# Kernel optimization log

Measured on AMD Instinct MI355X. Metric: run time of the kernel, lower is better.

## Reference

```python
import jax, jax.numpy as jnp
import numpy as np

B, C_IN, IMG, P = 64, 3, 224, 16
GRID = IMG // P              # 14
N_PATCH = GRID * GRID        # 196
S = N_PATCH + 1              # 197 tokens incl CLS
D, H, HD = 768, 12, 64
DFF = 3072
L, PRUNE_AFTER = 12, 4
RATIO, EPS = 0.5, 1e-6
NEG = -1e30                  # additive mask value (softmax weight -> exactly 0 in fp32)
N_CLASSES = 1000
N_KEEP = max(1, int(S * (1.0 - RATIO)))  # 98, matches torch topk count


def _ln(x, g, b):
    m = x.mean(-1, keepdims=True)
    v = ((x - m) ** 2).mean(-1, keepdims=True)
    return (x - m) * jax.lax.rsqrt(v + EPS) * g + b


def _attn(x, qkv_w, qkv_b, proj_w, proj_b, amask):
    Bx, N, C = x.shape
    qkv = (x @ qkv_w.T + qkv_b).reshape(Bx, N, 3, H, HD).transpose(2, 0, 3, 1, 4)
    q, k, v = qkv[0], qkv[1], qkv[2]            # [B,H,N,HD]
    s = jnp.einsum('bhqd,bhkd->bhqk', q, k) * (HD ** -0.5)
    if amask is not None:
        s = s + amask                            # [B,1,1,N] broadcast
    a = jax.nn.softmax(s, axis=-1)
    o = jnp.einsum('bhqk,bhkd->bhqd', a, v).transpose(0, 2, 1, 3).reshape(Bx, N, C)
    return o @ proj_w.T + proj_b


def _block(x, i, p, amask=None):
    h = _ln(x, p['ln1_g'][i], p['ln1_b'][i])
    x = x + _attn(h, p['qkv_w'][i], p['qkv_b'][i], p['proj_w'][i], p['proj_b'][i], amask)
    h = _ln(x, p['ln2_g'][i], p['ln2_b'][i])
    h = jax.nn.gelu(h @ p['fc1_w'][i].T + p['fc1_b'][i], approximate=False)
    x = x + (h @ p['fc2_w'][i].T + p['fc2_b'][i])
    return x


def _forward(images, patch_w, patch_b, cls_token, pos_embed,
             ln1_g, ln1_b, qkv_w, qkv_b, proj_w, proj_b,
             ln2_g, ln2_b, fc1_w, fc1_b, fc2_w, fc2_b,
             norm_g, norm_b, head_w, head_b):
    p = dict(ln1_g=ln1_g, ln1_b=ln1_b, qkv_w=qkv_w, qkv_b=qkv_b,
             proj_w=proj_w, proj_b=proj_b, ln2_g=ln2_g, ln2_b=ln2_b,
             fc1_w=fc1_w, fc1_b=fc1_b, fc2_w=fc2_w, fc2_b=fc2_b)
    Bx = images.shape[0]
    # patch embed: non-overlapping 16x16 conv == patch extract + matmul
    patches = images.reshape(Bx, C_IN, GRID, P, GRID, P).transpose(0, 2, 4, 1, 3, 5)
    patches = patches.reshape(Bx, N_PATCH, C_IN * P * P)
    x = patches @ patch_w.reshape(D, -1).T + patch_b          # [B,196,768]
    x = jnp.concatenate([jnp.broadcast_to(cls_token, (Bx, 1, D)), x], axis=1)
    x = x + pos_embed                                          # [B,197,768]
    # early dense blocks
    for i in range(PRUNE_AFTER):
        x = _block(x, i, p)
    # _threshold_prune: topk on token norms, CLS always kept
    scores = jnp.linalg.norm(x, axis=-1)                       # [B,S]
    _, idx = jax.lax.top_k(scores, N_KEEP)                     # [B,98]
    mask = jnp.zeros((Bx, S), bool).at[jnp.arange(Bx)[:, None], idx].set(True)
    mask = mask.at[:, 0].set(True)
    # _gather_pad: kept tokens compacted to front (original order), zeros after
    order = jnp.argsort(~mask, axis=1, stable=True)            # True positions first
    x_pad = jnp.take_along_axis(x, order[:, :, None], axis=1)
    attn_m = jnp.take_along_axis(mask, order, axis=1)          # [B,S] True-prefix
    x_pad = x_pad * attn_m[:, :, None]
    amask = jnp.where(attn_m, 0.0, NEG).astype(x.dtype)[:, None, None, :]  # [B,1,1,S]
    # late masked blocks
    for i in range(PRUNE_AFTER, L):
        x_pad = _block(x_pad, i, p, amask)
    cls = _ln(x_pad[:, 0], norm_g, norm_b)
    return cls @ head_w.T + head_b                             # [B,1000]


def setup_inputs():
    key = jax.random.key(0)
    ks = iter(jax.random.split(key, 32))
    r = lambda shape: jax.random.normal(next(ks), shape, jnp.float32) * 0.02
    return {
        'images': jax.random.normal(next(ks), (B, C_IN, IMG, IMG), jnp.float32),
        'patch_w': r((D, C_IN, P, P)),
        'patch_b': r((D,)),
        'cls_token': r((1, 1, D)),
        'pos_embed': r((1, S, D)),
        'ln1_g': jnp.ones((L, D), jnp.float32),
        'ln1_b': jnp.zeros((L, D), jnp.float32),
        'qkv_w': r((L, 3 * D, D)),
        'qkv_b': r((L, 3 * D)),
        'proj_w': r((L, D, D)),
        'proj_b': r((L, D)),
        'ln2_g': jnp.ones((L, D), jnp.float32),
        'ln2_b': jnp.zeros((L, D), jnp.float32),
        'fc1_w': r((L, DFF, D)),
        'fc1_b': r((L, DFF)),
        'fc2_w': r((L, D, DFF)),
        'fc2_b': r((L, D)),
        'norm_g': jnp.ones((D,), jnp.float32),
        'norm_b': jnp.zeros((D,), jnp.float32),
        'head_w': r((N_CLASSES, D)),
        'head_b': r((N_CLASSES,)),
    }


def reference(images, patch_w, patch_b, cls_token, pos_embed,
              ln1_g, ln1_b, qkv_w, qkv_b, proj_w, proj_b,
              ln2_g, ln2_b, fc1_w, fc1_b, fc2_w, fc2_b,
              norm_g, norm_b, head_w, head_b):
    return _forward(images, patch_w, patch_b, cls_token, pos_embed,
                    ln1_g, ln1_b, qkv_w, qkv_b, proj_w, proj_b,
                    ln2_g, ln2_b, fc1_w, fc1_b, fc2_w, fc2_b,
                    norm_g, norm_b, head_w, head_b)
```

## Files before the change

kernel.cpp:

```cpp
#include <hip/hip_runtime.h>
#include <cstdint>
#include <cstddef>


#define NTOK 197
#define NB 64
#define NHEAD 12
#define SL 99

typedef __attribute__((ext_vector_type(8))) _Float16 half8;
typedef __attribute__((ext_vector_type(4))) float f32x4;
typedef __attribute__((ext_vector_type(4))) unsigned short us4;

#define DEV static __device__ __forceinline__

DEV unsigned short f2h(float f) {
    union { _Float16 h; unsigned short u; } v;
    v.h = (_Float16)f;
    return v.u;
}
DEV float h2f(unsigned short u) {
    union { _Float16 h; unsigned short u; } v;
    v.u = u;
    return (float)v.h;
}

DEV void gload16(const void* g, void* l) {
    __builtin_amdgcn_global_load_lds((const __attribute__((address_space(1))) unsigned int*)g,
                                     (__attribute__((address_space(3))) unsigned int*)l, 16, 0, 0);
}

DEV float gelu_f(float v) {
    float x = v * 0.70710678118654752f;
    float ax = fabsf(x);
    float t = __builtin_amdgcn_rcpf(fmaf(0.3275911f, ax, 1.0f));
    float poly = fmaf(fmaf(fmaf(fmaf(1.061405429f, t, -1.453152027f), t,
                               1.421413741f), t, -0.284496736f), t, 0.254829592f) * t;
    float erf_ax = 1.0f - poly * __expf(-x * x);
    float er = (x < 0.f) ? -erf_ax : erf_ax;
    return 0.5f * v * (1.0f + er);
}

__global__ __launch_bounds__(256) void cvt_layer4_k(const float* __restrict__ qw,
                                                    const float* __restrict__ pw,
                                                    const float* __restrict__ f1,
                                                    const float* __restrict__ f2,
                                                    int i0,
                                                    unsigned short* __restrict__ dst)
{
    int l = blockIdx.x / 6912;
    int b2 = blockIdx.x % 6912;
    int li = i0 + l;
    size_t t = (size_t)b2 * 256 + threadIdx.x;
    size_t e = t * 4;
    const float* src; size_t loc;
    if (e < 1769472)      { src = qw + (size_t)li * 1769472; loc = e; }
    else if (e < 2359296) { src = pw + (size_t)li * 589824;  loc = e - 1769472; }
    else if (e < 4718592) { src = f1 + (size_t)li * 2359296; loc = e - 2359296; }
    else                  { src = f2 + (size_t)li * 2359296; loc = e - 4718592; }
    float4 v = *(const float4*)(src + loc);
    us4 hi; hi.x = f2h(v.x); hi.y = f2h(v.y); hi.z = f2h(v.z); hi.w = f2h(v.w);
    *(us4*)(dst + (size_t)l * 7077888 + e) = hi;
}

__global__ __launch_bounds__(256) void cvt_simple_k(const float* __restrict__ src,
                                                    unsigned short* __restrict__ dh, int n4)
{
    int t = blockIdx.x * 256 + threadIdx.x;
    if (t >= n4) return;
    size_t e = (size_t)t * 4;
    float4 v = *(const float4*)(src + e);
    us4 hi; hi.x = f2h(v.x); hi.y = f2h(v.y); hi.z = f2h(v.z); hi.w = f2h(v.w);
    *(us4*)(dh + e) = hi;
}

__global__ __launch_bounds__(256) void patch_extract2_k(const float* __restrict__ img,
                                                        unsigned short* __restrict__ ph)
{
    int pi = blockIdx.x, b = blockIdx.y;
    int gy = pi / 14, gx = pi % 14;
    size_t obase = ((size_t)b * 196 + pi) * 768;
    for (int f = threadIdx.x; f < 768; f += 256) {
        int c = f >> 8, py = (f >> 4) & 15, px = f & 15;
        float v = img[(((size_t)b * 3 + c) * 224 + gy * 16 + py) * 224 + gx * 16 + px];
        ph[obase + f] = f2h(v);
    }
}

__global__ __launch_bounds__(256) void assemble_k(const unsigned short* __restrict__ emb,
                                                  const float* __restrict__ cls,
                                                  const float* __restrict__ pos,
                                                  unsigned short* __restrict__ x)
{
    int s = blockIdx.x, b = blockIdx.y;
    size_t xo = ((size_t)b * NTOK + s) * 768;
    for (int d = threadIdx.x; d < 768; d += 256) {
        float v = (s == 0) ? cls[d] : h2f(emb[((size_t)b * 196 + (s - 1)) * 768 + d]);
        x[xo + d] = f2h(v + pos[(size_t)s * 768 + d]);
    }
}

__global__ __launch_bounds__(64) void lnw_k(const unsigned short* __restrict__ in,
                                            unsigned short* __restrict__ outh,
                                            const float* __restrict__ g,
                                            const float* __restrict__ bt, size_t ldin)
{
    const unsigned short* xr = in + (size_t)blockIdx.x * ldin;
    size_t ob = (size_t)blockIdx.x * 768;
    const int t = threadIdx.x;
    const int e0 = t * 12;

    us4 a = *(const us4*)(xr + e0);
    us4 b = *(const us4*)(xr + e0 + 4);
    us4 c = *(const us4*)(xr + e0 + 8);
    float v[12];
    v[0] = h2f(a.x); v[1] = h2f(a.y); v[2]  = h2f(a.z); v[3]  = h2f(a.w);
    v[4] = h2f(b.x); v[5] = h2f(b.y); v[6]  = h2f(b.z); v[7]  = h2f(b.w);
    v[8] = h2f(c.x); v[9] = h2f(c.y); v[10] = h2f(c.z); v[11] = h2f(c.w);

    float s = 0.f;
#pragma unroll
    for (int e = 0; e < 12; e++) s += v[e];
#pragma unroll
    for (int o = 32; o; o >>= 1) s += __shfl_xor(s, o);
    float mean = s * (1.f / 768.f);
    float ss = 0.f;
#pragma unroll
    for (int e = 0; e < 12; e++) { float d = v[e] - mean; ss += d * d; }
#pragma unroll
    for (int o = 32; o; o >>= 1) ss += __shfl_xor(ss, o);
    float inv = rsqrtf(ss * (1.f / 768.f) + 1e-6f);

    float4 g0 = *(const float4*)(g + e0),  g1 = *(const float4*)(g + e0 + 4),  g2 = *(const float4*)(g + e0 + 8);
    float4 b0 = *(const float4*)(bt + e0), b1 = *(const float4*)(bt + e0 + 4), b2 = *(const float4*)(bt + e0 + 8);
    float gg[12] = {g0.x,g0.y,g0.z,g0.w, g1.x,g1.y,g1.z,g1.w, g2.x,g2.y,g2.z,g2.w};
    float bb[12] = {b0.x,b0.y,b0.z,b0.w, b1.x,b1.y,b1.z,b1.w, b2.x,b2.y,b2.z,b2.w};
    unsigned short o16[12];
#pragma unroll
    for (int e = 0; e < 12; e++) o16[e] = f2h((v[e] - mean) * inv * gg[e] + bb[e]);
    us4 oa = {o16[0], o16[1], o16[2],  o16[3]};
    us4 obv = {o16[4], o16[5], o16[6],  o16[7]};
    us4 oc = {o16[8], o16[9], o16[10], o16[11]};
    *(us4*)(outh + ob + e0)     = oa;
    *(us4*)(outh + ob + e0 + 4) = obv;
    *(us4*)(outh + ob + e0 + 8) = oc;
}

template<int EPI, int OS, int MAP>
__global__ __launch_bounds__(256) void mgemm_k(const unsigned short* __restrict__ Ah,
                                               const unsigned short* __restrict__ Wh,
                                               const float* __restrict__ bias,
                                               const unsigned short* __restrict__ res,
                                               unsigned short* __restrict__ Chi,
                                               float* __restrict__ Cf,
                                               int M, int N, int K, int nR, int nC, int nRloc)
{
    __shared__ unsigned short lds[3 * 8192];

    int rt, ct;
    {
        int bid = blockIdx.x;
        if (MAP == 0) { rt = bid % nR; ct = bid / nR; }
        else {
            int xcd = bid & 7, u = bid >> 3, rl, c;
            if (MAP == 3) { rl = u % nRloc; c = u / nRloc; }
            else          { c = u % nC;     rl = u / nC;   }
            rt = xcd * nRloc + rl; ct = c;
            if (rt >= nR) return;
        }
    }
    const int row0 = rt << 7, col0 = ct << 7;
    const int tid = threadIdx.x;
    const int w = tid >> 6, lane = tid & 63;
    const int wr = w >> 1, wc = w & 1;
    const int srow = lane >> 2;
    const int schunk = ((lane & 3) ^ ((srow >> 1) & 3)) << 3;
    const int fr = lane & 15, fq = lane >> 4;
    const int rchunk = (fq ^ ((fr >> 1) & 3)) << 3;

    f32x4 acc[4][4];
#pragma unroll
    for (int m = 0; m < 4; m++)
#pragma unroll
        for (int n = 0; n < 4; n++) acc[m][n] = (f32x4)0.f;

    const int nk = K >> 5;

    auto stage = [&](int t, int slot) {
        const int k0 = t << 5;
        unsigned short* Ad = lds + slot * 8192;
        unsigned short* Bd = Ad + 4096;
#pragma unroll
        for (int i = 0; i < 2; i++) {
            int r = i * 64 + w * 16 + srow;
            int ga = row0 + r; if (ga > M - 1) ga = M - 1;
            int gb = col0 + r; if (gb > N - 1) gb = N - 1;
            gload16(Ah + (size_t)ga * K + k0 + schunk, Ad + i * 2048 + w * 512);
            gload16(Wh + (size_t)gb * K + k0 + schunk, Bd + i * 2048 + w * 512);
        }
    };

    stage(0, 0);
    stage(1, 1);
    int slot = 0, slot2 = 2;
    for (int t = 0; t < nk; ++t) {
        if (t + 1 < nk) asm volatile("s_waitcnt vmcnt(4)" ::: "memory");
        else            asm volatile("s_waitcnt vmcnt(0)" ::: "memory");
        __builtin_amdgcn_s_barrier();
        if (t + 2 < nk) stage(t + 2, slot2);
        const unsigned short* Ab = lds + slot * 8192;
        const unsigned short* Bb = Ab + 4096;
        half8 a[4], bb[4];
#pragma unroll
        for (int m = 0; m < 4; m++)
            a[m] = *(const half8*)(Ab + (wr * 64 + m * 16 + fr) * 32 + rchunk);
#pragma unroll
        for (int n = 0; n < 4; n++)
            bb[n] = *(const half8*)(Bb + (wc * 64 + n * 16 + fr) * 32 + rchunk);
#pragma unroll
        for (int m = 0; m < 4; m++)
#pragma unroll
            for (int n = 0; n < 4; n++)
                acc[m][n] = __builtin_amdgcn_mfma_f32_16x16x32_f16(a[m], bb[n], acc[m][n], 0, 0, 0);
        slot = (slot == 2) ? 0 : slot + 1;
        slot2 = (slot2 == 2) ? 0 : slot2 + 1;
    }

#pragma unroll
    for (int m = 0; m < 4; m++) {
#pragma unroll
        for (int n = 0; n < 4; n++) {
            int col = col0 + wc * 64 + n * 16 + fr;
#pragma unroll
            for (int r = 0; r < 4; r++) {
                int row = row0 + wr * 64 + m * 16 + fq * 4 + r;
                if (row < M && col < N) {
                    float v = acc[m][n][r] + bias[col];
                    size_t o = (size_t)row * N + col;
                    if (EPI == 2) v += h2f(res[o]);
                    if (EPI == 1) v = gelu_f(v);
                    if (OS == 0) Cf[o] = v;
                    else Chi[o] = f2h(v);
                }
            }
        }
    }
}

template<int S, int KT, int PVKT, int PSTR>
__global__ __launch_bounds__(256) void attn2_k(const unsigned short* __restrict__ qh,
                                               unsigned short* __restrict__ oh,
                                               const int* __restrict__ cntp)
{
    constexpr int PVK = PVKT * 32;
    constexpr int QT = (S + 15) / 16;
    extern __shared__ unsigned short sh[];
    unsigned short* VT = sh;
    unsigned short* PL = sh + 64 * PSTR;

    const int h = blockIdx.x, b = blockIdx.y;
    const int tid = threadIdx.x, w = tid >> 6, lane = tid & 63;
    const int nk = cntp ? cntp[b] : S;
    const size_t qbase = (size_t)b * S * 2304 + (size_t)h * 64;
    const int fr = lane & 15, fq = lane >> 4;

    for (int j0 = 0; j0 < S; j0 += 32) {
        int j = j0 + (tid >> 3);
        int d8 = (tid & 7) * 8;
        if (j < S) {
            size_t src = qbase + (size_t)j * 2304 + 1536 + d8;
            us4 v0 = *(const us4*)(qh + src);
            us4 v1 = *(const us4*)(qh + src + 4);
            VT[(d8 + 0) * PSTR + j] = v0.x; VT[(d8 + 1) * PSTR + j] = v0.y;
            VT[(d8 + 2) * PSTR + j] = v0.z; VT[(d8 + 3) * PSTR + j] = v0.w;
            VT[(d8 + 4) * PSTR + j] = v1.x; VT[(d8 + 5) * PSTR + j] = v1.y;
            VT[(d8 + 6) * PSTR + j] = v1.z; VT[(d8 + 7) * PSTR + j] = v1.w;
        }
    }
    for (int idx = tid; idx < 64 * (PVK - S); idx += 256) {
        int d = idx / (PVK - S), j = S + idx % (PVK - S);
        VT[d * PSTR + j] = 0;
    }
    {
        unsigned short* Pw = PL + w * 16 * PSTR;
        for (int idx = lane; idx < 16 * (PVK - 16 * KT); idx += 64) {
            int rr = idx / (PVK - 16 * KT), cc = 16 * KT + idx % (PVK - 16 * KT);
            Pw[rr * PSTR + cc] = 0;
        }
    }
    __syncthreads();

    for (int qt = w; qt < QT; qt += 4) {
        int qr = qt * 16 + fr; int qrc = qr < S ? qr : S - 1;
        const size_t qrow = qbase + (size_t)qrc * 2304;
        half8 qf0[2];
#pragma unroll
        for (int ks = 0; ks < 2; ks++)
            qf0[ks] = *(const half8*)(qh + qrow + ks * 32 + fq * 8);
        f32x4 sc[KT];
        __builtin_amdgcn_s_setprio(1);
#pragma unroll
        for (int kt = 0; kt < KT; kt++) {
            int ky = kt * 16 + fr; int kyc = ky < S ? ky : S - 1;
            const size_t krow = qbase + (size_t)kyc * 2304 + 768;
            f32x4 acc = (f32x4)0.f;
#pragma unroll
            for (int ks = 0; ks < 2; ks++) {
                half8 kh = *(const half8*)(qh + krow + ks * 32 + fq * 8);
                acc = __builtin_amdgcn_mfma_f32_16x16x32_f16(qf0[ks], kh, acc, 0, 0, 0);
            }
            sc[kt] = acc;
        }
        __builtin_amdgcn_s_setprio(0);
        float mx[4] = {-3e38f, -3e38f, -3e38f, -3e38f};
#pragma unroll
        for (int kt = 0; kt < KT; kt++) {
            bool valid = (kt * 16 + fr) < nk;
#pragma unroll
            for (int r = 0; r < 4; r++) {
                float s = sc[kt][r] * 0.125f;
                sc[kt][r] = s;
                if (valid) mx[r] = fmaxf(mx[r], s);
            }
        }
#pragma unroll
        for (int off = 1; off < 16; off <<= 1)
#pragma unroll
            for (int r = 0; r < 4; r++) mx[r] = fmaxf(mx[r], __shfl_xor(mx[r], off));
        float sum[4] = {0.f, 0.f, 0.f, 0.f};
#pragma unroll
        for (int kt = 0; kt < KT; kt++) {
            bool valid = (kt * 16 + fr) < nk;
#pragma unroll
            for (int r = 0; r < 4; r++) {
                float p = valid ? __expf(sc[kt][r] - mx[r]) : 0.f;
                sc[kt][r] = p;
                sum[r] += p;
            }
        }
#pragma unroll
        for (int off = 1; off < 16; off <<= 1)
#pragma unroll
            for (int r = 0; r < 4; r++) sum[r] += __shfl_xor(sum[r], off);
        float inv[4];
#pragma unroll
        for (int r = 0; r < 4; r++) inv[r] = 1.f / sum[r];
        unsigned short* Pw = PL + w * 16 * PSTR;
#pragma unroll
        for (int kt = 0; kt < KT; kt++) {
#pragma unroll
            for (int r = 0; r < 4; r++)
                Pw[(fq * 4 + r) * PSTR + kt * 16 + fr] = f2h(sc[kt][r] * inv[r]);
        }
        f32x4 o[4];
#pragma unroll
        for (int n = 0; n < 4; n++) o[n] = (f32x4)0.f;
        __builtin_amdgcn_s_setprio(1);
#pragma unroll
        for (int ks = 0; ks < PVKT; ks++) {
            half8 pa = *(const half8*)(Pw + fr * PSTR + ks * 32 + fq * 8);
#pragma unroll
            for (int n = 0; n < 4; n++) {
                half8 vb = *(const half8*)(VT + (n * 16 + fr) * PSTR + ks * 32 + fq * 8);
                o[n] = __builtin_amdgcn_mfma_f32_16x16x32_f16(pa, vb, o[n], 0, 0, 0);
            }
        }
        __builtin_amdgcn_s_setprio(0);
#pragma unroll
        for (int n = 0; n < 4; n++) {
#pragma unroll
            for (int r = 0; r < 4; r++) {
                int row = qt * 16 + fq * 4 + r;
                if (row < S) {
                    size_t oidx = ((size_t)b * S + row) * 768 + (size_t)h * 64 + n * 16 + fr;
                    oh[oidx] = f2h(o[n][r]);
                }
            }
        }
    }
}

__global__ __launch_bounds__(64) void normsq_k(const unsigned short* __restrict__ x,
                                               float* __restrict__ norms)
{
    const unsigned short* xr = x + (size_t)blockIdx.x * 768;
    const int t = threadIdx.x;
    const int e0 = t * 12;
    us4 a = *(const us4*)(xr + e0);
    us4 b = *(const us4*)(xr + e0 + 4);
    us4 c = *(const us4*)(xr + e0 + 8);
    float ss = 0.f;
    float v;
    v = h2f(a.x); ss += v * v; v = h2f(a.y); ss += v * v;
    v = h2f(a.z); ss += v * v; v = h2f(a.w); ss += v * v;
    v = h2f(b.x); ss += v * v; v = h2f(b.y); ss += v * v;
    v = h2f(b.z); ss += v * v; v = h2f(b.w); ss += v * v;
    v = h2f(c.x); ss += v * v; v = h2f(c.y); ss += v * v;
    v = h2f(c.z); ss += v * v; v = h2f(c.w); ss += v * v;
#pragma unroll
    for (int o = 32; o; o >>= 1) ss += __shfl_xor(ss, o);
    if (t == 0) norms[blockIdx.x] = ss;
}

__global__ __launch_bounds__(256) void topk_k(const float* __restrict__ norms,
                                              int* __restrict__ idxmap, int* __restrict__ cnt)
{
    int b = blockIdx.x, t = threadIdx.x;
    __shared__ float n[NTOK];
    __shared__ unsigned char kp[NTOK];
    if (t < NTOK) n[t] = norms[b * NTOK + t];
    __syncthreads();
    if (t < NTOK) {
        float me = n[t];
        int rank = 0;
        for (int j = 0; j < NTOK; j++) rank += (n[j] > me) || (n[j] == me && j < t);
        kp[t] = (rank < 98) || (t == 0);
    }
    __syncthreads();
    if (t == 0) {
        int c = 0;
        for (int s = 0; s < NTOK; s++) if (kp[s]) idxmap[b * SL + c++] = s;
        cnt[b] = c;
        for (int j = c; j < SL; j++) idxmap[b * SL + j] = 0;
    }
}

__global__ __launch_bounds__(64) void gather_k(const unsigned short* __restrict__ x,
                                               const int* __restrict__ idxmap,
                                               const int* __restrict__ cnt,
                                               unsigned short* __restrict__ xl)
{
    int j = blockIdx.x, b = blockIdx.y;
    size_t dst = ((size_t)b * SL + j) * 768;
    const int t = threadIdx.x;
    const int e0 = t * 12;
    if (j < cnt[b]) {
        int s = idxmap[b * SL + j];
        size_t src = ((size_t)b * NTOK + s) * 768;
        *(us4*)(xl + dst + e0)     = *(const us4*)(x + src + e0);
        *(us4*)(xl + dst + e0 + 4) = *(const us4*)(x + src + e0 + 4);
        *(us4*)(xl + dst + e0 + 8) = *(const us4*)(x + src + e0 + 8);
    } else {
        us4 z = {0, 0, 0, 0};
        *(us4*)(xl + dst + e0)     = z;
        *(us4*)(xl + dst + e0 + 4) = z;
        *(us4*)(xl + dst + e0 + 8) = z;
    }
}

extern "C" void kernel_launch(void* const* d_in, const int* in_sizes, int n_in,
                              void* d_out, int out_size, void* d_ws, size_t ws_size,
                              hipStream_t stream)
{
    const float* images  = (const float*)d_in[0];
    const float* patch_w = (const float*)d_in[1];
    const float* patch_b = (const float*)d_in[2];
    const float* cls_tok = (const float*)d_in[3];
    const float* pos_emb = (const float*)d_in[4];
    const float* ln1_g   = (const float*)d_in[5];
    const float* ln1_b   = (const float*)d_in[6];
    const float* qkv_w   = (const float*)d_in[7];
    const float* qkv_b   = (const float*)d_in[8];
    const float* proj_w  = (const float*)d_in[9];
    const float* proj_b  = (const float*)d_in[10];
    const float* ln2_g   = (const float*)d_in[11];
    const float* ln2_b   = (const float*)d_in[12];
    const float* fc1_w   = (const float*)d_in[13];
    const float* fc1_b   = (const float*)d_in[14];
    const float* fc2_w   = (const float*)d_in[15];
    const float* fc2_b   = (const float*)d_in[16];
    const float* norm_g  = (const float*)d_in[17];
    const float* norm_b  = (const float*)d_in[18];
    const float* head_w  = (const float*)d_in[19];
    const float* head_b  = (const float*)d_in[20];
    float* outp = (float*)d_out;

    char* W = (char*)d_ws;
    unsigned short* x16  = (unsigned short*)W;
    unsigned short* hbh  = (unsigned short*)(W + 19365888);
    char* R = W + 38731776;
    unsigned short* ph   = (unsigned short*)R;
    unsigned short* emb  = (unsigned short*)(R + 19365888);
    unsigned short* qkh  = (unsigned short*)R;
    unsigned short* ffh  = (unsigned short*)R;
    unsigned short* xl16 = (unsigned short*)(W + 116195328);
    unsigned short* wb4  = (unsigned short*)(W + 125927424);
    unsigned short* pwh  = (unsigned short*)(W + 182550528);
    unsigned short* hwb  = (unsigned short*)(W + 183730176);
    float* norms         = (float*)(W + 185303040);
    unsigned short* clsb = (unsigned short*)(W + 185353472);
    int* idxmap          = (int*)(W + 185451776);
    int* cnt             = (int*)(W + 185477120);

    const int LDS_EARLY = (64 * 232 + 4 * 16 * 232) * 2;
    const int LDS_LATE  = (64 * 136 + 4 * 16 * 136) * 2;
    (void)hipFuncSetAttribute(reinterpret_cast<const void*>(&attn2_k<197, 13, 7, 232>),
                              hipFuncAttributeMaxDynamicSharedMemorySize, LDS_EARLY);
    (void)hipFuncSetAttribute(reinterpret_cast<const void*>(&attn2_k<99, 7, 4, 136>),
                              hipFuncAttributeMaxDynamicSharedMemorySize, LDS_LATE);

    const int nR1 = 99, nRl1 = 13;
    const int nRp = 98, nRlp = 13;
    const int nR2 = 50, nRl2 = 7;

    cvt_simple_k<<<576, 256, 0, stream>>>(patch_w, pwh, 147456);
    patch_extract2_k<<<dim3(196, NB), 256, 0, stream>>>(images, ph);
    mgemm_k<0, 1, 3><<<8 * nRlp * 6, 256, 0, stream>>>(ph, pwh, patch_b, nullptr,
        emb, nullptr, 12544, 768, 768, nRp, 6, nRlp);
    assemble_k<<<dim3(NTOK, NB), 256, 0, stream>>>(emb, cls_tok, pos_emb, x16);

    const int M1 = NB * NTOK;
    for (int i = 0; i < 4; i++) {
        if (i == 0)
            cvt_layer4_k<<<4 * 6912, 256, 0, stream>>>(qkv_w, proj_w, fc1_w, fc2_w, 0, wb4);
        unsigned short* wbh = wb4 + (size_t)(i & 3) * 7077888;
        lnw_k<<<M1, 64, 0, stream>>>(x16, hbh, ln1_g + (size_t)i * 768, ln1_b + (size_t)i * 768, 768);
        mgemm_k<0, 1, 3><<<8 * nRl1 * 18, 256, 0, stream>>>(hbh, wbh,
            qkv_b + (size_t)i * 2304, nullptr, qkh, nullptr, M1, 2304, 768, nR1, 18, nRl1);
        attn2_k<197, 13, 7, 232><<<dim3(NHEAD, NB), 256, LDS_EARLY, stream>>>(qkh, hbh, nullptr);
        mgemm_k<2, 1, 3><<<8 * nRl1 * 6, 256, 0, stream>>>(hbh, wbh + 1769472,
            proj_b + (size_t)i * 768, x16, x16, nullptr, M1, 768, 768, nR1, 6, nRl1);
        lnw_k<<<M1, 64, 0, stream>>>(x16, hbh, ln2_g + (size_t)i * 768, ln2_b + (size_t)i * 768, 768);
        mgemm_k<1, 1, 3><<<8 * nRl1 * 24, 256, 0, stream>>>(hbh, wbh + 2359296,
            fc1_b + (size_t)i * 3072, nullptr, ffh, nullptr, M1, 3072, 768, nR1, 24, nRl1);
        mgemm_k<2, 1, 4><<<8 * nRl1 * 6, 256, 0, stream>>>(ffh, wbh + 4718592,
            fc2_b + (size_t)i * 768, x16, x16, nullptr, M1, 768, 3072, nR1, 6, nRl1);
    }

    normsq_k<<<M1, 64, 0, stream>>>(x16, norms);
    topk_k<<<NB, 256, 0, stream>>>(norms, idxmap, cnt);
    gather_k<<<dim3(SL, NB), 64, 0, stream>>>(x16, idxmap, cnt, xl16);

    const int M2 = NB * SL;
    for (int i = 4; i < 12; i++) {
        if (i == 4)
            cvt_layer4_k<<<4 * 6912, 256, 0, stream>>>(qkv_w, proj_w, fc1_w, fc2_w, 4, wb4);
        if (i == 8)
            cvt_layer4_k<<<4 * 6912, 256, 0, stream>>>(qkv_w, proj_w, fc1_w, fc2_w, 8, wb4);
        unsigned short* wbh = wb4 + (size_t)(i & 3) * 7077888;
        lnw_k<<<M2, 64, 0, stream>>>(xl16, hbh, ln1_g + (size_t)i * 768, ln1_b + (size_t)i * 768, 768);
        mgemm_k<0, 1, 3><<<8 * nRl2 * 18, 256, 0, stream>>>(hbh, wbh,
            qkv_b + (size_t)i * 2304, nullptr, qkh, nullptr, M2, 2304, 768, nR2, 18, nRl2);
        attn2_k<99, 7, 4, 136><<<dim3(NHEAD, NB), 256, LDS_LATE, stream>>>(qkh, hbh, cnt);
        mgemm_k<2, 1, 3><<<8 * nRl2 * 6, 256, 0, stream>>>(hbh, wbh + 1769472,
            proj_b + (size_t)i * 768, xl16, xl16, nullptr, M2, 768, 768, nR2, 6, nRl2);
        lnw_k<<<M2, 64, 0, stream>>>(xl16, hbh, ln2_g + (size_t)i * 768, ln2_b + (size_t)i * 768, 768);
        mgemm_k<1, 1, 3><<<8 * nRl2 * 24, 256, 0, stream>>>(hbh, wbh + 2359296,
            fc1_b + (size_t)i * 3072, nullptr, ffh, nullptr, M2, 3072, 768, nR2, 24, nRl2);
        mgemm_k<2, 1, 4><<<8 * nRl2 * 6, 256, 0, stream>>>(ffh, wbh + 4718592,
            fc2_b + (size_t)i * 768, xl16, xl16, nullptr, M2, 768, 3072, nR2, 6, nRl2);
    }

    lnw_k<<<NB, 64, 0, stream>>>(xl16, clsb, norm_g, norm_b, (size_t)SL * 768);
    cvt_simple_k<<<750, 256, 0, stream>>>(head_w, hwb, 192000);
    mgemm_k<0, 0, 0><<<8, 256, 0, stream>>>(clsb, hwb,
        head_b, nullptr, nullptr, outp, 64, 1000, 768, 1, 8, 1);
}
```

Measured before the change: 3.732 ms.

## Fold LayerNorm into QKV and FC1 GEMMs via weight scaling and row statistics

Removes the standalone LayerNorm kernels before the QKV and FC1 GEMMs. The gamma scale is folded into the fp16 weights during conversion, and per-column weight sums plus a beta/gamma-derived bias correction are precomputed. The GEMMs now consume the raw residual stream, accumulate per-row sum and sum-of-squares with fdot2 during the K loop, and apply mean/rstd correction in the epilogue. This saves a read and write of the normalized activations per LN, but adds dot ops to the inner loop and computes variance as E[x²]−mean², which can lose accuracy. The beta/gamma ratio is zero whenever gamma is zero.

```diff
diff --git a/kernel.cpp b/kernel.cpp
--- a/kernel.cpp
+++ b/kernel.cpp
@@ -9,6 +9,7 @@
 #define SL 99
 
 typedef __attribute__((ext_vector_type(8))) _Float16 half8;
+typedef __attribute__((ext_vector_type(2))) _Float16 half2;
 typedef __attribute__((ext_vector_type(4))) float f32x4;
 typedef __attribute__((ext_vector_type(4))) unsigned short us4;
 
@@ -41,10 +42,35 @@
     return 0.5f * v * (1.0f + er);
 }
 
+__global__ __launch_bounds__(256) void cvt_simple_k(const float* __restrict__ src,
+                                                    unsigned short* __restrict__ dh, int n4)
+{
+    int t = blockIdx.x * 256 + threadIdx.x;
+    if (t >= n4) return;
+    size_t e = (size_t)t * 4;
+    float4 v = *(const float4*)(src + e);
+    us4 hi; hi.x = f2h(v.x); hi.y = f2h(v.y); hi.z = f2h(v.z); hi.w = f2h(v.w);
+    *(us4*)(dh + e) = hi;
+}
+
+__global__ __launch_bounds__(256) void ratio_k(const float* __restrict__ ln1_g, const float* __restrict__ ln1_b,
+                                               const float* __restrict__ ln2_g, const float* __restrict__ ln2_b,
+                                               float* __restrict__ ratio)
+{
+    int idx = blockIdx.x * 256 + threadIdx.x;
+    if (idx >= 18432) return;
+    int l = idx / 1536, wh = (idx / 768) & 1, k = idx % 768;
+    float g = wh ? ln2_g[l * 768 + k] : ln1_g[l * 768 + k];
+    float b = wh ? ln2_b[l * 768 + k] : ln1_b[l * 768 + k];
+    ratio[idx] = (g != 0.f) ? b / g : 0.f;
+}
+
 __global__ __launch_bounds__(256) void cvt_layer4_k(const float* __restrict__ qw,
                                                     const float* __restrict__ pw,
                                                     const float* __restrict__ f1,
                                                     const float* __restrict__ f2,
+                                                    const float* __restrict__ ln1_g,
+                                                    const float* __restrict__ ln2_g,
                                                     int i0,
                                                     unsigned short* __restrict__ dst)
 {
@@ -54,24 +80,54 @@
     size_t t = (size_t)b2 * 256 + threadIdx.x;
     size_t e = t * 4;
     const float* src; size_t loc;
-    if (e < 1769472)      { src = qw + (size_t)li * 1769472; loc = e; }
+    const float* gsc = nullptr;
+    if (e < 1769472)      { src = qw + (size_t)li * 1769472; loc = e; gsc = ln1_g + (size_t)li * 768; }
     else if (e < 2359296) { src = pw + (size_t)li * 589824;  loc = e - 1769472; }
-    else if (e < 4718592) { src = f1 + (size_t)li * 2359296; loc = e - 2359296; }
+    else if (e < 4718592) { src = f1 + (size_t)li * 2359296; loc = e - 2359296; gsc = ln2_g + (size_t)li * 768; }
     else                  { src = f2 + (size_t)li * 2359296; loc = e - 4718592; }
     float4 v = *(const float4*)(src + loc);
+    if (gsc) {
+        int k = (int)(loc % 768);
+        float4 gv = *(const float4*)(gsc + k);
+        v.x *= gv.x; v.y *= gv.y; v.z *= gv.z; v.w *= gv.w;
+    }
     us4 hi; hi.x = f2h(v.x); hi.y = f2h(v.y); hi.z = f2h(v.z); hi.w = f2h(v.w);
     *(us4*)(dst + (size_t)l * 7077888 + e) = hi;
 }
 
-__global__ __launch_bounds__(256) void cvt_simple_k(const float* __restrict__ src,
-                                                    unsigned short* __restrict__ dh, int n4)
-{
-    int t = blockIdx.x * 256 + threadIdx.x;
-    if (t >= n4) return;
-    size_t e = (size_t)t * 4;
-    float4 v = *(const float4*)(src + e);
-    us4 hi; hi.x = f2h(v.x); hi.y = f2h(v.y); hi.z = f2h(v.z); hi.w = f2h(v.w);
-    *(us4*)(dh + e) = hi;
+__global__ __launch_bounds__(256) void sc_k(const unsigned short* __restrict__ wb4,
+                                            const float* __restrict__ ratio,
+                                            const float* __restrict__ qkv_b,
+                                            const float* __restrict__ fc1_b,
+                                            int i0,
+                                            float* __restrict__ sArr, float* __restrict__ cArr)
+{
+    int l = blockIdx.x / 1344;
+    int row = (blockIdx.x % 1344) * 4 + (threadIdx.x >> 6);
+    int lane = threadIdx.x & 63;
+    int li = i0 + l;
+    bool isq = row < 2304;
+    const unsigned short* wrow = wb4 + (size_t)l * 7077888 +
+        (isq ? (size_t)row * 768 : 2359296 + (size_t)(row - 2304) * 768);
+    const float* rat = ratio + ((size_t)li * 2 + (isq ? 0 : 1)) * 768;
+    float bias = isq ? qkv_b[(size_t)li * 2304 + row] : fc1_b[(size_t)li * 3072 + row - 2304];
+    int e0 = lane * 12;
+    us4 a = *(const us4*)(wrow + e0);
+    us4 b = *(const us4*)(wrow + e0 + 4);
+    us4 c = *(const us4*)(wrow + e0 + 8);
+    float4 r0 = *(const float4*)(rat + e0), r1 = *(const float4*)(rat + e0 + 4), r2 = *(const float4*)(rat + e0 + 8);
+    float v[12] = {h2f(a.x),h2f(a.y),h2f(a.z),h2f(a.w), h2f(b.x),h2f(b.y),h2f(b.z),h2f(b.w),
+                   h2f(c.x),h2f(c.y),h2f(c.z),h2f(c.w)};
+    float rr[12] = {r0.x,r0.y,r0.z,r0.w, r1.x,r1.y,r1.z,r1.w, r2.x,r2.y,r2.z,r2.w};
+    float s = 0.f, cc = 0.f;
+#pragma unroll
+    for (int e = 0; e < 12; e++) { s += v[e]; cc = fmaf(rr[e], v[e], cc); }
+#pragma unroll
+    for (int o = 32; o; o >>= 1) { s += __shfl_xor(s, o); cc += __shfl_xor(cc, o); }
+    if (lane == 0) {
+        sArr[(size_t)l * 5376 + row] = s;
+        cArr[(size_t)l * 5376 + row] = cc + bias;
+    }
 }
 
 __global__ __launch_bounds__(256) void patch_extract2_k(const float* __restrict__ img,
@@ -109,7 +165,6 @@
     size_t ob = (size_t)blockIdx.x * 768;
     const int t = threadIdx.x;
     const int e0 = t * 12;
-
     us4 a = *(const us4*)(xr + e0);
     us4 b = *(const us4*)(xr + e0 + 4);
     us4 c = *(const us4*)(xr + e0 + 8);
@@ -117,7 +172,6 @@
     v[0] = h2f(a.x); v[1] = h2f(a.y); v[2]  = h2f(a.z); v[3]  = h2f(a.w);
     v[4] = h2f(b.x); v[5] = h2f(b.y); v[6]  = h2f(b.z); v[7]  = h2f(b.w);
     v[8] = h2f(c.x); v[9] = h2f(c.y); v[10] = h2f(c.z); v[11] = h2f(c.w);
-
     float s = 0.f;
 #pragma unroll
     for (int e = 0; e < 12; e++) s += v[e];
@@ -130,7 +184,6 @@
 #pragma unroll
     for (int o = 32; o; o >>= 1) ss += __shfl_xor(ss, o);
     float inv = rsqrtf(ss * (1.f / 768.f) + 1e-6f);
-
     float4 g0 = *(const float4*)(g + e0),  g1 = *(const float4*)(g + e0 + 4),  g2 = *(const float4*)(g + e0 + 8);
     float4 b0 = *(const float4*)(bt + e0), b1 = *(const float4*)(bt + e0 + 4), b2 = *(const float4*)(bt + e0 + 8);
     float gg[12] = {g0.x,g0.y,g0.z,g0.w, g1.x,g1.y,g1.z,g1.w, g2.x,g2.y,g2.z,g2.w};
@@ -146,10 +199,11 @@
     *(us4*)(outh + ob + e0 + 8) = oc;
 }
 
-template<int EPI, int OS, int MAP>
+template<int EPI, int OS, int MAP, int LNF>
 __global__ __launch_bounds__(256) void mgemm_k(const unsigned short* __restrict__ Ah,
                                                const unsigned short* __restrict__ Wh,
                                                const float* __restrict__ bias,
+                                               const float* __restrict__ sArr,
                                                const unsigned short* __restrict__ res,
                                                unsigned short* __restrict__ Chi,
                                                float* __restrict__ Cf,
@@ -183,6 +237,10 @@
     for (int m = 0; m < 4; m++)
 #pragma unroll
         for (int n = 0; n < 4; n++) acc[m][n] = (f32x4)0.f;
+
+    float rs[4] = {0.f, 0.f, 0.f, 0.f};
+    float rq[4] = {0.f, 0.f, 0.f, 0.f};
+    const half2 one2 = {(_Float16)1.f, (_Float16)1.f};
 
     const int nk = K >> 5;
 
@@ -222,20 +280,57 @@
 #pragma unroll
             for (int n = 0; n < 4; n++)
                 acc[m][n] = __builtin_amdgcn_mfma_f32_16x16x32_f16(a[m], bb[n], acc[m][n], 0, 0, 0);
+        if (LNF) {
+#pragma unroll
+            for (int m = 0; m < 4; m++) {
+                const half2* p = (const half2*)&a[m];
+#pragma unroll
+                for (int j = 0; j < 4; j++) {
+                    rs[m] = __builtin_amdgcn_fdot2(p[j], one2, rs[m], false);
+                    rq[m] = __builtin_amdgcn_fdot2(p[j], p[j], rq[m], false);
+                }
+            }
+        }
         slot = (slot == 2) ? 0 : slot + 1;
         slot2 = (slot2 == 2) ? 0 : slot2 + 1;
     }
 
+    if (LNF) {
+#pragma unroll
+        for (int m = 0; m < 4; m++) {
+            rs[m] += __shfl_xor(rs[m], 16); rs[m] += __shfl_xor(rs[m], 32);
+            rq[m] += __shfl_xor(rq[m], 16); rq[m] += __shfl_xor(rq[m], 32);
+        }
+    }
+    const float invK = 1.f / (float)K;
+
 #pragma unroll
     for (int m = 0; m < 4; m++) {
+        float mean_r[4], rstd_r[4];
+        if (LNF) {
+#pragma unroll
+            for (int r = 0; r < 4; r++) {
+                int j = fq * 4 + r;
+                float sm = __shfl(rs[m], j);
+                float sq = __shfl(rq[m], j);
+                float mean = sm * invK;
+                float var = sq * invK - mean * mean;
+                mean_r[r] = mean;
+                rstd_r[r] = rsqrtf(var + 1e-6f);
+            }
+        }
 #pragma unroll
         for (int n = 0; n < 4; n++) {
             int col = col0 + wc * 64 + n * 16 + fr;
+            float sv = 0.f;
+            if (LNF && col < N) sv = sArr[col];
 #pragma unroll
             for (int r = 0; r < 4; r++) {
                 int row = row0 + wr * 64 + m * 16 + fq * 4 + r;
                 if (row < M && col < N) {
-                    float v = acc[m][n][r] + bias[col];
+                    float v;
+                    if (LNF) v = rstd_r[r] * (acc[m][n][r] - mean_r[r] * sv) + bias[col];
+                    else     v = acc[m][n][r] + bias[col];
                     size_t o = (size_t)row * N + col;
                     if (EPI == 2) v += h2f(res[o]);
                     if (EPI == 1) v = gelu_f(v);
@@ -491,6 +586,9 @@
     unsigned short* clsb = (unsigned short*)(W + 185353472);
     int* idxmap          = (int*)(W + 185451776);
     int* cnt             = (int*)(W + 185477120);
+    float* sArr          = (float*)(W + 185477632);
+    float* cArr          = (float*)(W + 185563648);
+    float* ratio         = (float*)(W + 185649664);
 
     const int LDS_EARLY = (64 * 232 + 4 * 16 * 232) * 2;
     const int LDS_LATE  = (64 * 136 + 4 * 16 * 136) * 2;
@@ -503,28 +601,32 @@
     const int nRp = 98, nRlp = 13;
     const int nR2 = 50, nRl2 = 7;
 
+    ratio_k<<<72, 256, 0, stream>>>(ln1_g, ln1_b, ln2_g, ln2_b, ratio);
+
     cvt_simple_k<<<576, 256, 0, stream>>>(patch_w, pwh, 147456);
     patch_extract2_k<<<dim3(196, NB), 256, 0, stream>>>(images, ph);
-    mgemm_k<0, 1, 3><<<8 * nRlp * 6, 256, 0, stream>>>(ph, pwh, patch_b, nullptr,
+    mgemm_k<0, 1, 3, 0><<<8 * nRlp * 6, 256, 0, stream>>>(ph, pwh, patch_b, nullptr, nullptr,
         emb, nullptr, 12544, 768, 768, nRp, 6, nRlp);
     assemble_k<<<dim3(NTOK, NB), 256, 0, stream>>>(emb, cls_tok, pos_emb, x16);
 
     const int M1 = NB * NTOK;
     for (int i = 0; i < 4; i++) {
-        if (i == 0)
-            cvt_layer4_k<<<4 * 6912, 256, 0, stream>>>(qkv_w, proj_w, fc1_w, fc2_w, 0, wb4);
+        if (i == 0) {
+            cvt_layer4_k<<<4 * 6912, 256, 0, stream>>>(qkv_w, proj_w, fc1_w, fc2_w, ln1_g, ln2_g, 0, wb4);
+            sc_k<<<4 * 1344, 256, 0, stream>>>(wb4, ratio, qkv_b, fc1_b, 0, sArr, cArr);
+        }
         unsigned short* wbh = wb4 + (size_t)(i & 3) * 7077888;
-        lnw_k<<<M1, 64, 0, stream>>>(x16, hbh, ln1_g + (size_t)i * 768, ln1_b + (size_t)i * 768, 768);
-        mgemm_k<0, 1, 3><<<8 * nRl1 * 18, 256, 0, stream>>>(hbh, wbh,
-            qkv_b + (size_t)i * 2304, nullptr, qkh, nullptr, M1, 2304, 768, nR1, 18, nRl1);
+        float* sL = sArr + (size_t)(i & 3) * 5376;
+        float* cL = cArr + (size_t)(i & 3) * 5376;
+        mgemm_k<0, 1, 3, 1><<<8 * nRl1 * 18, 256, 0, stream>>>(x16, wbh,
+            cL, sL, nullptr, qkh, nullptr, M1, 2304, 768, nR1, 18, nRl1);
         attn2_k<197, 13, 7, 232><<<dim3(NHEAD, NB), 256, LDS_EARLY, stream>>>(qkh, hbh, nullptr);
-        mgemm_k<2, 1, 3><<<8 * nRl1 * 6, 256, 0, stream>>>(hbh, wbh + 1769472,
-            proj_b + (size_t)i * 768, x16, x16, nullptr, M1, 768, 768, nR1, 6, nRl1);
-        lnw_k<<<M1, 64, 0, stream>>>(x16, hbh, ln2_g + (size_t)i * 768, ln2_b + (size_t)i * 768, 768);
-        mgemm_k<1, 1, 3><<<8 * nRl1 * 24, 256, 0, stream>>>(hbh, wbh + 2359296,
-            fc1_b + (size_t)i * 3072, nullptr, ffh, nullptr, M1, 3072, 768, nR1, 24, nRl1);
-        mgemm_k<2, 1, 4><<<8 * nRl1 * 6, 256, 0, stream>>>(ffh, wbh + 4718592,
-            fc2_b + (size_t)i * 768, x16, x16, nullptr, M1, 768, 3072, nR1, 6, nRl1);
+        mgemm_k<2, 1, 3, 0><<<8 * nRl1 * 6, 256, 0, stream>>>(hbh, wbh + 1769472,
+            proj_b + (size_t)i * 768, nullptr, x16, x16, nullptr, M1, 768, 768, nR1, 6, nRl1);
+        mgemm_k<1, 1, 3, 1><<<8 * nRl1 * 24, 256, 0, stream>>>(x16, wbh + 2359296,
+            cL + 2304, sL + 2304, nullptr, ffh, nullptr, M1, 3072, 768, nR1, 24, nRl1);
+        mgemm_k<2, 1, 4, 0><<<8 * nRl1 * 6, 256, 0, stream>>>(ffh, wbh + 4718592,
+            fc2_b + (size_t)i * 768, nullptr, x16, x16, nullptr, M1, 768, 3072, nR1, 6, nRl1);
     }
 
     normsq_k<<<M1, 64, 0, stream>>>(x16, norms);
@@ -533,26 +635,30 @@
 
     const int M2 = NB * SL;
     for (int i = 4; i < 12; i++) {
-        if (i == 4)
-            cvt_layer4_k<<<4 * 6912, 256, 0, stream>>>(qkv_w, proj_w, fc1_w, fc2_w, 4, wb4);
-        if (i == 8)
-            cvt_layer4_k<<<4 * 6912, 256, 0, stream>>>(qkv_w, proj_w, fc1_w, fc2_w, 8, wb4);
+        if (i == 4) {
+            cvt_layer4_k<<<4 * 6912, 256, 0, stream>>>(qkv_w, proj_w, fc1_w, fc2_w, ln1_g, ln2_g, 4, wb4);
+            sc_k<<<4 * 1344, 256, 0, stream>>>(wb4, ratio, qkv_b, fc1_b, 4, sArr, cArr);
+        }
+        if (i == 8) {
+            cvt_layer4_k<<<4 * 6912, 256, 0, stream>>>(qkv_w, proj_w, fc1_w, fc2_w, ln1_g, ln2_g, 8, wb4);
+            sc_k<<<4 * 1344, 256, 0, stream>>>(wb4, ratio, qkv_b, fc1_b, 8, sArr, cArr);
+        }
         unsigned short* wbh = wb4 + (size_t)(i & 3) * 7077888;
-        lnw_k<<<M2, 64, 0, stream>>>(xl16, hbh, ln1_g + (size_t)i * 768, ln1_b + (size_t)i * 768, 768);
-        mgemm_k<0, 1, 3><<<8 * nRl2 * 18, 256, 0, stream>>>(hbh, wbh,
-            qkv_b + (size_t)i * 2304, nullptr, qkh, nullptr, M2, 2304, 768, nR2, 18, nRl2);
+        float* sL = sArr + (size_t)(i & 3) * 5376;
+        float* cL = cArr + (size_t)(i & 3) * 5376;
+        mgemm_k<0, 1, 3, 1><<<8 * nRl2 * 18, 256, 0, stream>>>(xl16, wbh,
+            cL, sL, nullptr, qkh, nullptr, M2, 2304, 768, nR2, 18, nRl2);
         attn2_k<99, 7, 4, 136><<<dim3(NHEAD, NB), 256, LDS_LATE, stream>>>(qkh, hbh, cnt);
-        mgemm_k<2, 1, 3><<<8 * nRl2 * 6, 256, 0, stream>>>(hbh, wbh + 1769472,
-            proj_b + (size_t)i * 768, xl16, xl16, nullptr, M2, 768, 768, nR2, 6, nRl2);
-        lnw_k<<<M2, 64, 0, stream>>>(xl16, hbh, ln2_g + (size_t)i * 768, ln2_b + (size_t)i * 768, 768);
-        mgemm_k<1, 1, 3><<<8 * nRl2 * 24, 256, 0, stream>>>(hbh, wbh + 2359296,
-            fc1_b + (size_t)i * 3072, nullptr, ffh, nullptr, M2, 3072, 768, nR2, 24, nRl2);
-        mgemm_k<2, 1, 4><<<8 * nRl2 * 6, 256, 0, stream>>>(ffh, wbh + 4718592,
-            fc2_b + (size_t)i * 768, xl16, xl16, nullptr, M2, 768, 3072, nR2, 6, nRl2);
+        mgemm_k<2, 1, 3, 0><<<8 * nRl2 * 6, 256, 0, stream>>>(hbh, wbh + 1769472,
+            proj_b + (size_t)i * 768, nullptr, xl16, xl16, nullptr, M2, 768, 768, nR2, 6, nRl2);
+        mgemm_k<1, 1, 3, 1><<<8 * nRl2 * 24, 256, 0, stream>>>(xl16, wbh + 2359296,
+            cL + 2304, sL + 2304, nullptr, ffh, nullptr, M2, 3072, 768, nR2, 24, nRl2);
+        mgemm_k<2, 1, 4, 0><<<8 * nRl2 * 6, 256, 0, stream>>>(ffh, wbh + 4718592,
+            fc2_b + (size_t)i * 768, nullptr, xl16, xl16, nullptr, M2, 768, 3072, nR2, 6, nRl2);
     }
 
     lnw_k<<<NB, 64, 0, stream>>>(xl16, clsb, norm_g, norm_b, (size_t)SL * 768);
     cvt_simple_k<<<750, 256, 0, stream>>>(head_w, hwb, 192000);
-    mgemm_k<0, 0, 0><<<8, 256, 0, stream>>>(clsb, hwb,
-        head_b, nullptr, nullptr, outp, 64, 1000, 768, 1, 8, 1);
-}
+    mgemm_k<0, 0, 0, 0><<<8, 256, 0, stream>>>(clsb, hwb,
+        head_b, nullptr, nullptr, nullptr, outp, 64, 1000, 768, 1, 8, 1);
+}
```

After: 3.756 ms. No clear change (+0.6%).
